# Performance work log

Measured on AMD Instinct MI355X. Metric: run time of the kernel, lower is better.

Reference implementation:

```python
import jax, jax.numpy as jnp
import numpy as np
from jax import lax

# Model dims (match init_kwargs / input_specs)
B, T, N_IN, N_MID, N_OUT = 256, 100, 784, 1024, 10
L_TAU = 0.8  # state decay


def setup_inputs() -> dict:
    key = jax.random.key(0)
    ks = jax.random.split(key, 10)
    x = jax.random.uniform(ks[0], (B, T, N_IN), dtype=jnp.float32)  # input spikes/rates
    y = jax.random.randint(ks[1], (B,), 0, N_OUT, dtype=jnp.int64)

    def lin(k, fan_in, fan_out):
        return jax.random.normal(k, (fan_in, fan_out), dtype=jnp.float32) / np.sqrt(fan_in)

    return {
        "x": x, "y": y,
        "W1": lin(ks[2], N_IN, N_MID),  "b1": jnp.zeros((N_MID,), jnp.float32),
        "W2": lin(ks[3], N_MID, N_MID), "b2": jnp.zeros((N_MID,), jnp.float32),
        "W3": lin(ks[4], N_MID, N_MID), "b3": jnp.zeros((N_MID,), jnp.float32),
        "W4": lin(ks[5], N_MID, N_OUT), "b4": jnp.zeros((N_OUT,), jnp.float32),
    }


def _snu(s, y_prev, x_in, W, b):
    # SNU cell (soft): s_t = relu(W x_t + tau * s_{t-1} * (1 - y_{t-1})); y_t = sigmoid(s_t + b)
    s = jax.nn.relu(x_in @ W + L_TAU * s * (1.0 - y_prev))
    y_out = jax.nn.sigmoid(s + b)
    return s, y_out


def reference(x, y, W1, b1, W2, b2, W3, b3, W4, b4):
    bsz = x.shape[0]
    zeros = lambda n: jnp.zeros((bsz, n), x.dtype)
    carry0 = (zeros(N_MID), zeros(N_MID), zeros(N_MID), zeros(N_MID),
              zeros(N_MID), zeros(N_MID), zeros(N_OUT), zeros(N_OUT))

    def step(carry, x_t):
        s1, y1, s2, y2, s3, y3, s4, y4 = carry
        s1, y1 = _snu(s1, y1, x_t, W1, b1)
        s2, y2 = _snu(s2, y2, y1, W2, b2)
        s3, y3 = _snu(s3, y3, y2, W3, b3)
        s4, y4 = _snu(s4, y4, y3, W4, b4)
        return (s1, y1, s2, y2, s3, y3, s4, y4), y4

    xs = jnp.transpose(x, (1, 0, 2))  # [T, B, n_in]
    _, outs = lax.scan(step, carry0, xs)  # outs: [T, B, n_out]
    # out_rec also stacked the initial zero output; it contributes 0 to the sum
    m = jnp.sum(outs, axis=0)  # [B, n_out]
    logp = jax.nn.log_softmax(m, axis=-1)
    loss = -jnp.mean(jnp.take_along_axis(logp, y[:, None], axis=1))
    return loss, m
```

## Files before the change

kernel.cpp:

```cpp
#include <hip/hip_runtime.h>
#include <hip/hip_bf16.h>


#define BDIM 256
#define TT   100
#define TP   112
#define BB   256
#define MM2  (BB * TP)
#define NMID 1024
#define K1   784
#define K1P  896
#define NOUT 10
#define N4P  16
#define L_TAU 0.8f

#define NBLK 256
#define ZST  102

#define PB_CX   1024
#define PB_TC1  (PB_CX + 896)
#define PB_TC23 (PB_TC1 + 2048)
#define PB_W4   (PB_TC23 + 16)

typedef __attribute__((ext_vector_type(4))) int   int4x;
typedef __attribute__((ext_vector_type(8))) int   int8x;
typedef __attribute__((ext_vector_type(4))) float f32x4;

__device__ __forceinline__ void async_copy16(const void* g, void* l) {
    __builtin_amdgcn_global_load_lds(
        (const __attribute__((address_space(1))) unsigned int*)g,
        (__attribute__((address_space(3))) unsigned int*)l,
        16, 0, 0);
}

__device__ __forceinline__ unsigned short f2bf(float f) {
    __hip_bfloat16 h = __float2bfloat16(f);
    return __builtin_bit_cast(unsigned short, h);
}
__device__ __forceinline__ float bf2f(unsigned short u) {
    return __uint_as_float((unsigned)u << 16);
}

__device__ __forceinline__ void tc_body(const float* __restrict__ W,
                                        unsigned char* __restrict__ WT,
                                        int K, int N, int Kpad,
                                        int bx, int by, int tidx) {
    __shared__ float tile[32][33];
    int k0 = bx * 32;
    int n0 = by * 32;
    int tx = tidx & 31, ty = tidx >> 5;
    #pragma unroll
    for (int i = 0; i < 4; ++i) {
        int k = k0 + ty + i * 8;
        tile[ty + i * 8][tx] = (k < K) ? W[(long)k * N + n0 + tx] : 0.0f;
    }
    __syncthreads();
    int nl = tidx >> 3, kq = tidx & 7;
    int pk = __builtin_amdgcn_cvt_pk_fp8_f32(tile[kq * 4 + 0][nl], tile[kq * 4 + 1][nl], 0, false);
    pk     = __builtin_amdgcn_cvt_pk_fp8_f32(tile[kq * 4 + 2][nl], tile[kq * 4 + 3][nl], pk, true);
    *(int*)(WT + (long)(n0 + nl) * Kpad + k0 + kq * 4) = pk;
}

__global__ __launch_bounds__(256) void prep_fused(
    const float* __restrict__ X,  unsigned char* __restrict__ XB,
    const float* __restrict__ W1, unsigned char* __restrict__ W1T,
    const float* __restrict__ W2, unsigned char* __restrict__ W2T,
    const float* __restrict__ W3, unsigned char* __restrict__ W3T,
    const float* __restrict__ W4, unsigned char* __restrict__ W4T)
{
    const int bid = blockIdx.x;
    const int th  = threadIdx.x;

    if (bid < PB_CX) {
        int b = bid >> 2;
        int q = bid & 3;
        if (th >= K1P / 4) return;
        const float4* xs = (const float4*)(X + ((long)b * TT + q * 25) * K1);
        unsigned char* xd = XB + ((long)b * TP + q * 25) * K1P;
        for (int tt = 0; tt < 25; ++tt) {
            int pk = 0;
            if (th < K1 / 4) {
                float4 v = xs[(long)tt * (K1 / 4) + th];
                pk = __builtin_amdgcn_cvt_pk_fp8_f32(v.x, v.y, 0, false);
                pk = __builtin_amdgcn_cvt_pk_fp8_f32(v.z, v.w, pk, true);
            }
            *(int*)(xd + (long)tt * K1P + th * 4) = pk;
        }
    } else if (bid < PB_TC1) {
        int idx = bid - PB_CX;
        tc_body(W1, W1T, K1, NMID, K1P, idx % 28, idx / 28, th);
    } else if (bid < PB_TC23) {
        int idx = bid - PB_TC1;
        int z   = idx >> 10;
        int rem = idx & 1023;
        tc_body(z ? W3 : W2, z ? W3T : W2T, NMID, NMID, NMID,
                rem & 31, rem >> 5, th);
    } else {
        int idx = bid - PB_TC23;
        int tid = idx * BDIM + th;
        int n = tid >> 8;
        int k4 = (tid & 255) * 4;
        float v0 = 0, v1 = 0, v2 = 0, v3 = 0;
        if (n < NOUT) {
            v0 = W4[(k4 + 0) * NOUT + n];
            v1 = W4[(k4 + 1) * NOUT + n];
            v2 = W4[(k4 + 2) * NOUT + n];
            v3 = W4[(k4 + 3) * NOUT + n];
        }
        int pk = __builtin_amdgcn_cvt_pk_fp8_f32(v0, v1, 0, false);
        pk     = __builtin_amdgcn_cvt_pk_fp8_f32(v2, v3, pk, true);
        *(int*)(W4T + (long)n * NMID + k4) = pk;
    }
}

__device__ __forceinline__ void stage_tile(const unsigned char* Aptr,
                                           const unsigned char* Bptr,
                                           unsigned char* As, unsigned char* Bs,
                                           int srow, int lch, int Kp, int k0) {
    #pragma unroll
    for (int i = 0; i < 4; ++i)
        if (srow + i * 32 < TP)
            async_copy16(Aptr + (long)(i * 32) * Kp + k0,
                         &As[(srow + i * 32) * 128 + lch * 16]);
    #pragma unroll
    for (int i = 0; i < 8; ++i)
        async_copy16(Bptr + (long)(i * 32) * Kp + k0,
                     &Bs[(srow + i * 32) * 128 + lch * 16]);
}

__global__ __launch_bounds__(256, 3) void gemm_snu_fused(
    const unsigned char* __restrict__ A,
    const unsigned char* __restrict__ BT,
    const float* __restrict__ bias,
    unsigned char* __restrict__ Y,
    int Kp)
{
    __shared__ unsigned char smem[52224];
    unsigned char* As = smem;
    unsigned char* Bs = smem + 14336;
    unsigned short* Zs = (unsigned short*)smem;

    const int tid  = threadIdx.x;
    const int wave = tid >> 6;
    const int lane = tid & 63;

    const int l   = blockIdx.x;
    const int xcd = l & 7;
    const int p   = l >> 3;
    const int b   = xcd * 32 + (p >> 2);
    const int bn  = (p & 3) * NBLK;

    const long arow0 = (long)b * TP;

    const float bv = bias[bn + tid];
    unsigned char* yp = Y + arow0 * NMID + bn + tid;

    f32x4 acc[7][4] = {};

    const int srow = tid >> 3;
    const int lch  = tid & 7;
    const int gch  = lch ^ (srow & 7);
    const unsigned char* Aptr = A  + (arow0 + srow) * Kp + gch * 16;
    const unsigned char* Bptr = BT + (long)(bn + srow) * Kp + gch * 16;

    const int mrow = lane & 15;
    const int g    = lane >> 4;
    const int wc   = wave * 64;

    for (int k0 = 0; k0 < Kp; k0 += 128) {
        stage_tile(Aptr, Bptr, As, Bs, srow, lch, Kp, k0);
        __syncthreads();

        int8x bfr[4];
        #pragma unroll
        for (int j = 0; j < 4; ++j) {
            int row = wc + j * 16 + mrow;
            int r7  = row & 7;
            int4x lo = *(const int4x*)&Bs[row * 128 + ((2 * g    ) ^ r7) * 16];
            int4x hi = *(const int4x*)&Bs[row * 128 + ((2 * g + 1) ^ r7) * 16];
            bfr[j][0] = lo[0]; bfr[j][1] = lo[1]; bfr[j][2] = lo[2]; bfr[j][3] = lo[3];
            bfr[j][4] = hi[0]; bfr[j][5] = hi[1]; bfr[j][6] = hi[2]; bfr[j][7] = hi[3];
        }
        #pragma unroll
        for (int i = 0; i < 7; ++i) {
            int row = i * 16 + mrow;
            int r7  = row & 7;
            int4x lo = *(const int4x*)&As[row * 128 + ((2 * g    ) ^ r7) * 16];
            int4x hi = *(const int4x*)&As[row * 128 + ((2 * g + 1) ^ r7) * 16];
            int8x af;
            af[0] = lo[0]; af[1] = lo[1]; af[2] = lo[2]; af[3] = lo[3];
            af[4] = hi[0]; af[5] = hi[1]; af[6] = hi[2]; af[7] = hi[3];
            #pragma unroll
            for (int j = 0; j < 4; ++j)
                acc[i][j] = __builtin_amdgcn_mfma_scale_f32_16x16x128_f8f6f4(
                    bfr[j], af, acc[i][j],
                    0, 0,
                    0, 0x7F,
                    0, 0x7F);
        }
        __syncthreads();
    }

    #pragma unroll
    for (int i = 0; i < 7; ++i)
        #pragma unroll
        for (int j = 0; j < 4; ++j) {
            int t  = i * 16 + mrow;
            int nn = wc + j * 16 + g * 4;
            if (t < TT)
                #pragma unroll
                for (int r = 0; r < 4; ++r)
                    Zs[(nn + r) * ZST + t] = f2bf(acc[i][j][r]);
        }
    __syncthreads();

    {
        const unsigned short* zp = Zs + tid * ZST;
        float s = 0.0f, u = 1.0f;
        unsigned int zc = *(const unsigned int*)(zp);
        unsigned int z1 = *(const unsigned int*)(zp + 2);
        for (int t0 = 0; t0 < TT; t0 += 2) {
            unsigned int z2 = 0;
            if (t0 + 4 < TT) z2 = *(const unsigned int*)(zp + t0 + 4);
            float z = bf2f((unsigned short)(zc & 0xFFFFu));
            s = fmaxf(fmaf(L_TAU * s, u, z), 0.0f);
            u = __builtin_amdgcn_rcpf(1.0f + __expf(s + bv));
            yp[(long)t0 * NMID] = (unsigned char)(__builtin_amdgcn_cvt_pk_fp8_f32(1.0f - u, 0.0f, 0, false) & 0xFF);
            z = bf2f((unsigned short)(zc >> 16));
            s = fmaxf(fmaf(L_TAU * s, u, z), 0.0f);
            u = __builtin_amdgcn_rcpf(1.0f + __expf(s + bv));
            yp[(long)(t0 + 1) * NMID] = (unsigned char)(__builtin_amdgcn_cvt_pk_fp8_f32(1.0f - u, 0.0f, 0, false) & 0xFF);
            zc = z1; z1 = z2;
        }
    }
}

__global__ __launch_bounds__(256) void layer4_fused(
    const unsigned char* __restrict__ Y3,
    const unsigned char* __restrict__ W4T,
    const float* __restrict__ b4,
    float* __restrict__ m_out)
{
    __shared__ float Z4s[TP][N4P];

    const int tid  = threadIdx.x;
    const int wave = tid >> 6;
    const int lane = tid & 63;
    const int mrow = lane & 15;
    const int g    = lane >> 4;
    const int b    = blockIdx.x;

    int8x wf[8];
    {
        const unsigned char* wp = W4T + (long)mrow * NMID + g * 32;
        #pragma unroll
        for (int kt = 0; kt < 8; ++kt) {
            int4x wlo = *(const int4x*)(wp + kt * 128);
            int4x whi = *(const int4x*)(wp + kt * 128 + 16);
            wf[kt][0] = wlo[0]; wf[kt][1] = wlo[1]; wf[kt][2] = wlo[2]; wf[kt][3] = wlo[3];
            wf[kt][4] = whi[0]; wf[kt][5] = whi[1]; wf[kt][6] = whi[2]; wf[kt][7] = whi[3];
        }
    }

    for (int rg = wave; rg < 7; rg += 4) {
        const long row = (long)b * TP + rg * 16 + mrow;
        const unsigned char* ap = Y3 + row * NMID + g * 32;
        f32x4 acc = {};
        #pragma unroll
        for (int kt = 0; kt < 8; ++kt) {
            int4x alo = *(const int4x*)(ap + kt * 128);
            int4x ahi = *(const int4x*)(ap + kt * 128 + 16);
            int8x af;
            af[0] = alo[0]; af[1] = alo[1]; af[2] = alo[2]; af[3] = alo[3];
            af[4] = ahi[0]; af[5] = ahi[1]; af[6] = ahi[2]; af[7] = ahi[3];
            acc = __builtin_amdgcn_mfma_scale_f32_16x16x128_f8f6f4(
                wf[kt], af, acc, 0, 0, 0, 0x7F, 0, 0x7F);
        }
        *(f32x4*)&Z4s[rg * 16 + mrow][g * 4] = acc;
    }
    __syncthreads();

    if (tid < NOUT) {
        const float bv = b4[tid];
        float s = 0.0f, u = 1.0f, msum = 0.0f;
        float zc = Z4s[0][tid];
        float z1 = Z4s[1][tid];
        for (int t = 0; t < TT; ++t) {
            float z2 = (t + 2 < TT) ? Z4s[t + 2][tid] : 0.0f;
            s = fmaxf(fmaf(L_TAU * s, u, zc), 0.0f);
            u = __builtin_amdgcn_rcpf(1.0f + __expf(s + bv));
            msum += 1.0f - u;
            zc = z1; z1 = z2;
        }
        m_out[b * NOUT + tid] = msum;
    }
}

__global__ void loss_kernel(const float* __restrict__ m, const int* __restrict__ y,
                            float* __restrict__ out) {
    __shared__ float red[BDIM];
    int b = threadIdx.x;
    float v[NOUT];
    float mx = -1e30f;
    #pragma unroll
    for (int n = 0; n < NOUT; ++n) { v[n] = m[b * NOUT + n]; mx = fmaxf(mx, v[n]); }
    float se = 0.0f;
    #pragma unroll
    for (int n = 0; n < NOUT; ++n) se += __expf(v[n] - mx);
    float lse = mx + __logf(se);
    int lbl = y[b];
    float vy = 0.0f;
    #pragma unroll
    for (int n = 0; n < NOUT; ++n) if (n == lbl) vy = v[n];
    red[b] = -(vy - lse);
    __syncthreads();
    for (int off = 128; off; off >>= 1) {
        if (b < off) red[b] += red[b + off];
        __syncthreads();
    }
    if (b == 0) out[0] = red[0] / (float)BB;
}

extern "C" void kernel_launch(void* const* d_in, const int* in_sizes, int n_in,
                              void* d_out, int out_size, void* d_ws, size_t ws_size,
                              hipStream_t stream) {
    const float* x  = (const float*)d_in[0];
    const int*   y  = (const int*)  d_in[1];
    const float* W1 = (const float*)d_in[2];
    const float* b1 = (const float*)d_in[3];
    const float* W2 = (const float*)d_in[4];
    const float* b2 = (const float*)d_in[5];
    const float* W3 = (const float*)d_in[6];
    const float* b3 = (const float*)d_in[7];
    const float* W4 = (const float*)d_in[8];
    const float* b4 = (const float*)d_in[9];
    float* out = (float*)d_out;

    char* ws = (char*)d_ws;
    size_t off = 0;
    auto alloc = [&](size_t bytes) {
        char* p = ws + off;
        off = (off + bytes + 255) & ~(size_t)255;
        return (void*)p;
    };
    unsigned char* XB  = (unsigned char*)alloc((size_t)MM2 * K1P);
    unsigned char* W1T = (unsigned char*)alloc((size_t)NMID * K1P);
    unsigned char* W2T = (unsigned char*)alloc((size_t)NMID * NMID);
    unsigned char* W3T = (unsigned char*)alloc((size_t)NMID * NMID);
    unsigned char* W4T = (unsigned char*)alloc((size_t)N4P * NMID);
    unsigned char* Ya  = (unsigned char*)alloc((size_t)MM2 * NMID);
    unsigned char* Yb  = (unsigned char*)alloc((size_t)MM2 * NMID);

    prep_fused<<<PB_W4, BDIM, 0, stream>>>(x, XB, W1, W1T, W2, W2T, W3, W3T, W4, W4T);

    const int fblocks = BB * (NMID / NBLK);
    gemm_snu_fused<<<fblocks, BDIM, 0, stream>>>(XB, W1T, b1, Ya, K1P);
    gemm_snu_fused<<<fblocks, BDIM, 0, stream>>>(Ya, W2T, b2, Yb, NMID);
    gemm_snu_fused<<<fblocks, BDIM, 0, stream>>>(Yb, W3T, b3, Ya, NMID);
    layer4_fused<<<BB, BDIM, 0, stream>>>(Ya, W4T, b4, out + 1);
    loss_kernel<<<1, BDIM, 0, stream>>>(out + 1, y, out);
}
```

Before: 333.3 us.

## Halve shared-memory footprint by staging B tile in two passes for higher occupancy

The fused GEMM+SNU kernel now loads the 256-column B tile in two 128-row halves that reuse one shared buffer, and keeps all seven A fragments in registers across both halves. The recurrence epilogue is also split into two passes of 128 columns, so the Z staging buffer shrinks. Together this cuts LDS from about 52KB to 30KB and raises the launch-bounds occupancy target from 3 to 5 blocks. The cost is two extra barriers per k-step, serialized B loads with less overlap, only half the threads active in each epilogue pass, and more register pressure from holding A fragments.

```diff
diff --git a/kernel.cpp b/kernel.cpp
--- a/kernel.cpp
+++ b/kernel.cpp
@@ -113,29 +113,14 @@
     }
 }
 
-__device__ __forceinline__ void stage_tile(const unsigned char* Aptr,
-                                           const unsigned char* Bptr,
-                                           unsigned char* As, unsigned char* Bs,
-                                           int srow, int lch, int Kp, int k0) {
-    #pragma unroll
-    for (int i = 0; i < 4; ++i)
-        if (srow + i * 32 < TP)
-            async_copy16(Aptr + (long)(i * 32) * Kp + k0,
-                         &As[(srow + i * 32) * 128 + lch * 16]);
-    #pragma unroll
-    for (int i = 0; i < 8; ++i)
-        async_copy16(Bptr + (long)(i * 32) * Kp + k0,
-                     &Bs[(srow + i * 32) * 128 + lch * 16]);
-}
-
-__global__ __launch_bounds__(256, 3) void gemm_snu_fused(
+__global__ __launch_bounds__(256, 5) void gemm_snu_fused(
     const unsigned char* __restrict__ A,
     const unsigned char* __restrict__ BT,
     const float* __restrict__ bias,
     unsigned char* __restrict__ Y,
     int Kp)
 {
-    __shared__ unsigned char smem[52224];
+    __shared__ unsigned char smem[30720];
     unsigned char* As = smem;
     unsigned char* Bs = smem + 14336;
     unsigned short* Zs = (unsigned short*)smem;
@@ -152,8 +137,11 @@
 
     const long arow0 = (long)b * TP;
 
-    const float bv = bias[bn + tid];
-    unsigned char* yp = Y + arow0 * NMID + bn + tid;
+    const int ntl = bn + (tid & 127);
+    const float bvlo = bias[ntl];
+    const float bvhi = bias[ntl + 128];
+    unsigned char* ypl = Y + arow0 * NMID + ntl;
+    unsigned char* yph = ypl + 128;
 
     f32x4 acc[7][4] = {};
 
@@ -165,73 +153,112 @@
 
     const int mrow = lane & 15;
     const int g    = lane >> 4;
-    const int wc   = wave * 64;
+    const int wc2  = wave * 32;
 
     for (int k0 = 0; k0 < Kp; k0 += 128) {
-        stage_tile(Aptr, Bptr, As, Bs, srow, lch, Kp, k0);
-        __syncthreads();
-
-        int8x bfr[4];
-        #pragma unroll
-        for (int j = 0; j < 4; ++j) {
-            int row = wc + j * 16 + mrow;
-            int r7  = row & 7;
-            int4x lo = *(const int4x*)&Bs[row * 128 + ((2 * g    ) ^ r7) * 16];
-            int4x hi = *(const int4x*)&Bs[row * 128 + ((2 * g + 1) ^ r7) * 16];
-            bfr[j][0] = lo[0]; bfr[j][1] = lo[1]; bfr[j][2] = lo[2]; bfr[j][3] = lo[3];
-            bfr[j][4] = hi[0]; bfr[j][5] = hi[1]; bfr[j][6] = hi[2]; bfr[j][7] = hi[3];
-        }
+        #pragma unroll
+        for (int i = 0; i < 4; ++i)
+            if (srow + i * 32 < TP)
+                async_copy16(Aptr + (long)(i * 32) * Kp + k0,
+                             &As[(srow + i * 32) * 128 + lch * 16]);
+        #pragma unroll
+        for (int i = 0; i < 4; ++i)
+            async_copy16(Bptr + (long)(i * 32) * Kp + k0,
+                         &Bs[(srow + i * 32) * 128 + lch * 16]);
+        __syncthreads();
+
+        int8x af[7];
         #pragma unroll
         for (int i = 0; i < 7; ++i) {
             int row = i * 16 + mrow;
             int r7  = row & 7;
             int4x lo = *(const int4x*)&As[row * 128 + ((2 * g    ) ^ r7) * 16];
             int4x hi = *(const int4x*)&As[row * 128 + ((2 * g + 1) ^ r7) * 16];
-            int8x af;
-            af[0] = lo[0]; af[1] = lo[1]; af[2] = lo[2]; af[3] = lo[3];
-            af[4] = hi[0]; af[5] = hi[1]; af[6] = hi[2]; af[7] = hi[3];
+            af[i][0] = lo[0]; af[i][1] = lo[1]; af[i][2] = lo[2]; af[i][3] = lo[3];
+            af[i][4] = hi[0]; af[i][5] = hi[1]; af[i][6] = hi[2]; af[i][7] = hi[3];
+        }
+
+        int8x bfr[2];
+        #pragma unroll
+        for (int jj = 0; jj < 2; ++jj) {
+            int row = wc2 + jj * 16 + mrow;
+            int r7  = row & 7;
+            int4x lo = *(const int4x*)&Bs[row * 128 + ((2 * g    ) ^ r7) * 16];
+            int4x hi = *(const int4x*)&Bs[row * 128 + ((2 * g + 1) ^ r7) * 16];
+            bfr[jj][0] = lo[0]; bfr[jj][1] = lo[1]; bfr[jj][2] = lo[2]; bfr[jj][3] = lo[3];
+            bfr[jj][4] = hi[0]; bfr[jj][5] = hi[1]; bfr[jj][6] = hi[2]; bfr[jj][7] = hi[3];
+        }
+        #pragma unroll
+        for (int i = 0; i < 7; ++i)
             #pragma unroll
-            for (int j = 0; j < 4; ++j)
-                acc[i][j] = __builtin_amdgcn_mfma_scale_f32_16x16x128_f8f6f4(
-                    bfr[j], af, acc[i][j],
-                    0, 0,
-                    0, 0x7F,
-                    0, 0x7F);
-        }
-        __syncthreads();
-    }
-
-    #pragma unroll
-    for (int i = 0; i < 7; ++i)
-        #pragma unroll
-        for (int j = 0; j < 4; ++j) {
-            int t  = i * 16 + mrow;
-            int nn = wc + j * 16 + g * 4;
-            if (t < TT)
-                #pragma unroll
-                for (int r = 0; r < 4; ++r)
-                    Zs[(nn + r) * ZST + t] = f2bf(acc[i][j][r]);
-        }
-    __syncthreads();
-
-    {
-        const unsigned short* zp = Zs + tid * ZST;
-        float s = 0.0f, u = 1.0f;
-        unsigned int zc = *(const unsigned int*)(zp);
-        unsigned int z1 = *(const unsigned int*)(zp + 2);
-        for (int t0 = 0; t0 < TT; t0 += 2) {
-            unsigned int z2 = 0;
-            if (t0 + 4 < TT) z2 = *(const unsigned int*)(zp + t0 + 4);
-            float z = bf2f((unsigned short)(zc & 0xFFFFu));
-            s = fmaxf(fmaf(L_TAU * s, u, z), 0.0f);
-            u = __builtin_amdgcn_rcpf(1.0f + __expf(s + bv));
-            yp[(long)t0 * NMID] = (unsigned char)(__builtin_amdgcn_cvt_pk_fp8_f32(1.0f - u, 0.0f, 0, false) & 0xFF);
-            z = bf2f((unsigned short)(zc >> 16));
-            s = fmaxf(fmaf(L_TAU * s, u, z), 0.0f);
-            u = __builtin_amdgcn_rcpf(1.0f + __expf(s + bv));
-            yp[(long)(t0 + 1) * NMID] = (unsigned char)(__builtin_amdgcn_cvt_pk_fp8_f32(1.0f - u, 0.0f, 0, false) & 0xFF);
-            zc = z1; z1 = z2;
-        }
+            for (int jj = 0; jj < 2; ++jj)
+                acc[i][jj] = __builtin_amdgcn_mfma_scale_f32_16x16x128_f8f6f4(
+                    bfr[jj], af[i], acc[i][jj],
+                    0, 0, 0, 0x7F, 0, 0x7F);
+        __syncthreads();
+
+        #pragma unroll
+        for (int i = 0; i < 4; ++i)
+            async_copy16(Bptr + (long)(128 + i * 32) * Kp + k0,
+                         &Bs[(srow + i * 32) * 128 + lch * 16]);
+        __syncthreads();
+
+        #pragma unroll
+        for (int jj = 0; jj < 2; ++jj) {
+            int row = wc2 + jj * 16 + mrow;
+            int r7  = row & 7;
+            int4x lo = *(const int4x*)&Bs[row * 128 + ((2 * g    ) ^ r7) * 16];
+            int4x hi = *(const int4x*)&Bs[row * 128 + ((2 * g + 1) ^ r7) * 16];
+            bfr[jj][0] = lo[0]; bfr[jj][1] = lo[1]; bfr[jj][2] = lo[2]; bfr[jj][3] = lo[3];
+            bfr[jj][4] = hi[0]; bfr[jj][5] = hi[1]; bfr[jj][6] = hi[2]; bfr[jj][7] = hi[3];
+        }
+        #pragma unroll
+        for (int i = 0; i < 7; ++i)
+            #pragma unroll
+            for (int jj = 0; jj < 2; ++jj)
+                acc[i][2 + jj] = __builtin_amdgcn_mfma_scale_f32_16x16x128_f8f6f4(
+                    bfr[jj], af[i], acc[i][2 + jj],
+                    0, 0, 0, 0x7F, 0, 0x7F);
+        __syncthreads();
+    }
+
+    #pragma unroll
+    for (int h = 0; h < 2; ++h) {
+        #pragma unroll
+        for (int i = 0; i < 7; ++i)
+            #pragma unroll
+            for (int jj = 0; jj < 2; ++jj) {
+                int t  = i * 16 + mrow;
+                int nn = wc2 + jj * 16 + g * 4;
+                if (t < TT)
+                    #pragma unroll
+                    for (int r = 0; r < 4; ++r)
+                        Zs[(nn + r) * ZST + t] = f2bf(acc[i][2 * h + jj][r]);
+            }
+        __syncthreads();
+
+        if (tid < 128) {
+            const float bv = h ? bvhi : bvlo;
+            unsigned char* yp = h ? yph : ypl;
+            const unsigned short* zp = Zs + tid * ZST;
+            float s = 0.0f, u = 1.0f;
+            unsigned int zc = *(const unsigned int*)(zp);
+            unsigned int z1 = *(const unsigned int*)(zp + 2);
+            for (int t0 = 0; t0 < TT; t0 += 2) {
+                unsigned int z2 = 0;
+                if (t0 + 4 < TT) z2 = *(const unsigned int*)(zp + t0 + 4);
+                float z = bf2f((unsigned short)(zc & 0xFFFFu));
+                s = fmaxf(fmaf(L_TAU * s, u, z), 0.0f);
+                u = __builtin_amdgcn_rcpf(1.0f + __expf(s + bv));
+                yp[(long)t0 * NMID] = (unsigned char)(__builtin_amdgcn_cvt_pk_fp8_f32(1.0f - u, 0.0f, 0, false) & 0xFF);
+                z = bf2f((unsigned short)(zc >> 16));
+                s = fmaxf(fmaf(L_TAU * s, u, z), 0.0f);
+                u = __builtin_amdgcn_rcpf(1.0f + __expf(s + bv));
+                yp[(long)(t0 + 1) * NMID] = (unsigned char)(__builtin_amdgcn_cvt_pk_fp8_f32(1.0f - u, 0.0f, 0, false) & 0xFF);
+                zc = z1; z1 = z2;
+            }
+        }
+        __syncthreads();
     }
 }
 
```

Result: slower. 1.152 ms (+245.7%).
